# Kernel tuning notes

Measured on AMD Instinct MI355X. Metric: run time of the kernel, lower is better.

Reference implementation:

```python
import jax, jax.numpy as jnp
import numpy as np

B, L = 2, 2048
D_MODEL = 1024; D_STATE = 128; D_CONV = 4; EXPAND = 2; HEADDIM = 64
D_HALF = D_MODEL // 2
D_INNER = EXPAND * D_HALF           # 1024
NHEADS = D_INNER // HEADDIM         # 16
CONV_DIM = D_INNER + 2 * D_STATE    # 1280 (x, B, C share the depthwise conv)
D_IN_PROJ = 2 * D_INNER + 2 * D_STATE + NHEADS  # 2320 (z, xBC, dt)
EPS = 1e-5


def _rmsnorm(x, w):
    return x * jax.lax.rsqrt(jnp.mean(x * x, axis=-1, keepdims=True) + EPS) * w


def _mamba2(u, in_w, conv_w, conv_b, dt_bias, A_log, D, gnorm_w, outp_w):
    """Mamba2 block (ngroups=1, rmsnorm gated, no proj biases), u: [b,l,D_HALF]."""
    b, l, _ = u.shape
    zxbcdt = u @ in_w.T                                # [b,l,D_IN_PROJ]
    z = zxbcdt[..., :D_INNER]
    xBC = zxbcdt[..., D_INNER:D_INNER + CONV_DIM]
    dt = zxbcdt[..., D_INNER + CONV_DIM:]              # [b,l,h]
    # causal depthwise conv1d (kernel D_CONV) + silu
    xp = jnp.pad(xBC, ((0, 0), (D_CONV - 1, 0), (0, 0)))
    conv = conv_b + sum(xp[:, k:k + l, :] * conv_w[:, k] for k in range(D_CONV))
    xBC = jax.nn.silu(conv)
    x = xBC[..., :D_INNER]
    Bm = xBC[..., D_INNER:D_INNER + D_STATE]           # [b,l,n]
    Cm = xBC[..., D_INNER + D_STATE:]                  # [b,l,n]
    dt = jax.nn.softplus(dt + dt_bias)                 # [b,l,h]
    A = -jnp.exp(A_log)                                # [h]
    xh = x.reshape(b, l, NHEADS, HEADDIM)              # [b,l,h,p]
    dA = jnp.exp(dt * A)                               # [b,l,h]
    dtx = dt[..., None] * xh                           # [b,l,h,p]

    def step(h, inp):
        dA_t, dtx_t, B_t, C_t = inp
        h = dA_t[:, :, None, None] * h + jnp.einsum('bhp,bn->bhpn', dtx_t, B_t)
        return h, jnp.einsum('bhpn,bn->bhp', h, C_t)

    h0 = jnp.zeros((b, NHEADS, HEADDIM, D_STATE), u.dtype)
    xs = (jnp.moveaxis(dA, 1, 0), jnp.moveaxis(dtx, 1, 0),
          jnp.moveaxis(Bm, 1, 0), jnp.moveaxis(Cm, 1, 0))
    _, ys = jax.lax.scan(step, h0, xs)                 # ys: [l,b,h,p]
    y = jnp.moveaxis(ys, 0, 1) + xh * D[None, None, :, None]
    y = y.reshape(b, l, D_INNER) * jax.nn.silu(z)      # gate, then gated RMSNorm
    y = _rmsnorm(y, gnorm_w)
    return y @ outp_w.T                                # [b,l,D_HALF]


def _forward(x, norm_w, op_w, op_b,
             f_in_w, f_conv_w, f_conv_b, f_dt_bias, f_A_log, f_D, f_gnorm_w, f_outp_w,
             b_in_w, b_conv_w, b_conv_b, b_dt_bias, b_A_log, b_D, b_gnorm_w, b_outp_w):
    xn = _rmsnorm(x, norm_w)
    x_f, x_b = xn[..., :D_HALF], xn[..., D_HALF:]
    out_f = _mamba2(x_f, f_in_w, f_conv_w, f_conv_b, f_dt_bias, f_A_log, f_D, f_gnorm_w, f_outp_w)
    out_b = jnp.flip(
        _mamba2(jnp.flip(x_b, 1), b_in_w, b_conv_w, b_conv_b, b_dt_bias, b_A_log, b_D, b_gnorm_w, b_outp_w), 1)
    out = jnp.concatenate([out_f, out_b], axis=-1) @ op_w.T + op_b
    return x + out


def _mamba_params(key, prefix):
    k = jax.random.split(key, 5)
    return {
        prefix + 'in_w': jax.random.normal(k[0], (D_IN_PROJ, D_HALF), jnp.float32) * 0.02,
        prefix + 'conv_w': jax.random.normal(k[1], (CONV_DIM, D_CONV), jnp.float32) * 0.2,
        prefix + 'conv_b': jnp.zeros((CONV_DIM,), jnp.float32),
        prefix + 'dt_bias': jax.random.normal(k[2], (NHEADS,), jnp.float32) * 0.1,
        prefix + 'A_log': jnp.log(jax.random.uniform(k[3], (NHEADS,), jnp.float32, 1.0, 16.0)),
        prefix + 'D': jnp.ones((NHEADS,), jnp.float32),
        prefix + 'gnorm_w': jnp.ones((D_INNER,), jnp.float32),
        prefix + 'outp_w': jax.random.normal(k[4], (D_HALF, D_INNER), jnp.float32) * 0.02,
    }


def setup_inputs():
    key = jax.random.key(0)
    k = jax.random.split(key, 4)
    inp = {
        'x': jax.random.normal(k[0], (B, L, D_MODEL), jnp.float32),
        'norm_w': jnp.ones((D_MODEL,), jnp.float32),
        'op_w': jax.random.normal(k[1], (D_MODEL, D_MODEL), jnp.float32) * 0.02,
        'op_b': jnp.zeros((D_MODEL,), jnp.float32),
    }
    inp.update(_mamba_params(k[2], 'f_'))
    inp.update(_mamba_params(k[3], 'b_'))
    return inp


def reference(x, norm_w, op_w, op_b,
              f_in_w, f_conv_w, f_conv_b, f_dt_bias, f_A_log, f_D, f_gnorm_w, f_outp_w,
              b_in_w, b_conv_w, b_conv_b, b_dt_bias, b_A_log, b_D, b_gnorm_w, b_outp_w):
    return _forward(x, norm_w, op_w, op_b,
                    f_in_w, f_conv_w, f_conv_b, f_dt_bias, f_A_log, f_D, f_gnorm_w, f_outp_w,
                    b_in_w, b_conv_w, b_conv_b, b_dt_bias, b_A_log, b_D, b_gnorm_w, b_outp_w)
```

## Files before the change

### kernel.cpp

```cpp
#include <hip/hip_runtime.h>
#include <math.h>

#define L_SEQ   2048
#define NBATCH  2
#define DMODEL  1024
#define DHALF   512
#define DINNER  1024
#define DSTATE  128
#define NHEADS  16
#define HEADDIM 64
#define CONVDIM 1280
#define DINPROJ 2320
#define ROWS    4096
#define NPADIN  2432

#define QCH     64
#define NCH     (L_SEQ / QCH)

typedef __attribute__((ext_vector_type(8))) short bf16x8;
typedef __attribute__((ext_vector_type(4))) float f32x4;

union US8 { uint4 q; unsigned short s[8]; };
union US4 { uint2 q; unsigned short s[4]; };

__device__ __forceinline__ float siluf(float v){ return v / (1.f + expf(-v)); }
__device__ __forceinline__ float softplusf(float v){ return v > 20.f ? v : log1pf(expf(v)); }
__device__ __forceinline__ unsigned short f2bf(float f){
  union { float f; unsigned u; } x; x.f = f;
  unsigned r = (x.u + 0x7fffu + ((x.u >> 16) & 1u)) >> 16;
  return (unsigned short)r;
}
__device__ __forceinline__ float bf2f(unsigned short u){
  union { unsigned u; float f; } x; x.u = ((unsigned)u) << 16; return x.f;
}
__device__ __forceinline__ void gload16(const void* g, void* l){
  __builtin_amdgcn_global_load_lds((const __attribute__((address_space(1))) void*)g,
                                   (__attribute__((address_space(3))) void*)l, 16, 0, 0);
}
__device__ __forceinline__ int kx(int row){ return ((row ^ (row >> 3)) & 7) << 3; }

__device__ __forceinline__ float blockReduceSum256(float v, float* red){
  #pragma unroll
  for (int o = 32; o > 0; o >>= 1) v += __shfl_xor(v, o);
  int wid = threadIdx.x >> 6, lane = threadIdx.x & 63;
  if (lane == 0) red[wid] = v;
  __syncthreads();
  return red[0] + red[1] + red[2] + red[3];
}

__global__ void rmsnorm_split_kernel(const float* __restrict__ x, const float* __restrict__ nw,
                                     unsigned short* __restrict__ uf, unsigned short* __restrict__ ub){
  __shared__ float red[4];
  int row = blockIdx.x;
  int tid = threadIdx.x;
  float4 v4 = *(const float4*)(x + (size_t)row*DMODEL + tid*4);
  float ss = v4.x*v4.x + v4.y*v4.y + v4.z*v4.z + v4.w*v4.w;
  ss = blockReduceSum256(ss, red);
  float scale = rsqrtf(ss * (1.f/DMODEL) + 1e-5f);
  int t = row & (L_SEQ-1);
  int fliprow = (row ^ t) | (L_SEQ-1-t);
  float4 w4 = *(const float4*)(nw + tid*4);
  US4 o;
  o.s[0] = f2bf(v4.x*scale*w4.x);
  o.s[1] = f2bf(v4.y*scale*w4.y);
  o.s[2] = f2bf(v4.z*scale*w4.z);
  o.s[3] = f2bf(v4.w*scale*w4.w);
  int d = tid*4;
  if (d < DHALF) *(uint2*)&uf[(size_t)row*DHALF + d] = o.q;
  else           *(uint2*)&ub[(size_t)fliprow*DHALF + (d - DHALF)] = o.q;
}

__global__ void wconv_all_kernel(const float* __restrict__ s0, const float* __restrict__ s1,
                                 const float* __restrict__ s2, const float* __restrict__ s3,
                                 const float* __restrict__ s4,
                                 unsigned short* __restrict__ d0, unsigned short* __restrict__ d1,
                                 unsigned short* __restrict__ d2, unsigned short* __restrict__ d3,
                                 unsigned short* __restrict__ d4){
  const int S01 = NPADIN*DHALF;
  const int S23 = DHALF*DINNER;
  const int S4  = DMODEL*DMODEL;
  int idx = blockIdx.x*256 + threadIdx.x;
  if (idx < S01){
    int row = idx >> 9;
    d0[idx] = (row < DINPROJ) ? f2bf(s0[idx]) : (unsigned short)0;
    return;
  }
  idx -= S01;
  if (idx < S01){
    int row = idx >> 9;
    d1[idx] = (row < DINPROJ) ? f2bf(s1[idx]) : (unsigned short)0;
    return;
  }
  idx -= S01;
  if (idx < S23){ d2[idx] = f2bf(s2[idx]); return; }
  idx -= S23;
  if (idx < S23){ d3[idx] = f2bf(s3[idx]); return; }
  idx -= S23;
  if (idx < S4){ d4[idx] = f2bf(s4[idx]); }
}

__global__ __launch_bounds__(256) void gemm_bf16_kernel(
    const unsigned short* __restrict__ A0, const unsigned short* __restrict__ A1, int lda,
    const unsigned short* __restrict__ W0, const unsigned short* __restrict__ W1,
    float* __restrict__ Cf, int ldc,
    const float* __restrict__ bias, const float* __restrict__ res,
    unsigned short* __restrict__ O0a, unsigned short* __restrict__ O0b, int ld0,
    unsigned short* __restrict__ O1a, unsigned short* __restrict__ O1b, int n1, int ld1,
    float* __restrict__ O2a, float* __restrict__ O2b, int n2, int ld2,
    int coff1, int flip1,
    int M, int Nreal, int K){
  __shared__ unsigned short As[2][128*32];
  __shared__ unsigned short Bs[2][128*32];
  int bid = (blockIdx.z*gridDim.y + blockIdx.y)*gridDim.x + blockIdx.x;
  int nwg = gridDim.x*gridDim.y*gridDim.z;
  int s = bid;
  if ((nwg & 7) == 0){
    int cpx = nwg >> 3;
    s = (bid & 7)*cpx + (bid >> 3);
  }
  int bx = s % gridDim.x;
  int tmp = s / gridDim.x;
  int by = tmp % gridDim.y;
  int dir = tmp / gridDim.y;

  const unsigned short* A = dir ? A1 : A0;
  const unsigned short* W = dir ? W1 : W0;
  unsigned short* O0 = dir ? O0b : O0a;
  unsigned short* O1 = dir ? O1b : O1a;
  float* O2 = dir ? O2b : O2a;
  int coff = dir ? coff1 : 0;
  int flip = dir ? flip1 : 0;

  int bm = by*128, bn = bx*128;
  int tid = threadIdx.x;
  int lane = tid & 63;
  int wave = tid >> 6;
  int wm = (wave >> 1) * 64, wn = (wave & 1) * 64;
  int l15 = lane & 15, lhi = lane >> 4;
  f32x4 acc[4][4];
  #pragma unroll
  for (int i = 0; i < 4; i++)
    #pragma unroll
    for (int j = 0; j < 4; j++)
      acc[i][j] = (f32x4){0.f,0.f,0.f,0.f};

  auto stage = [&](int bufi, int k0){
    #pragma unroll
    for (int j = 0; j < 2; j++){
      int f = j*256 + tid;
      int row = f >> 2, c8 = (f & 3) * 8;
      gload16(A + (size_t)(bm+row)*lda + k0 + c8, &As[bufi][f*8]);
      gload16(W + (size_t)(bn+row)*K   + k0 + c8, &Bs[bufi][f*8]);
    }
  };

  stage(0, 0);
  __syncthreads();
  int cur = 0;
  for (int k0 = 0; k0 < K; k0 += 32){
    if (k0 + 32 < K) stage(cur ^ 1, k0 + 32);
    bf16x8 af[4], bfr[4];
    #pragma unroll
    for (int i = 0; i < 4; i++){
      af[i]  = *(const bf16x8*)&As[cur][(wm + i*16 + l15)*32 + lhi*8];
      bfr[i] = *(const bf16x8*)&Bs[cur][(wn + i*16 + l15)*32 + lhi*8];
    }
    #pragma unroll
    for (int i = 0; i < 4; i++)
      #pragma unroll
      for (int j = 0; j < 4; j++)
        acc[i][j] = __builtin_amdgcn_mfma_f32_16x16x32_bf16(af[i], bfr[j], acc[i][j], 0, 0, 0);
    __syncthreads();
    cur ^= 1;
  }
  #pragma unroll
  for (int i = 0; i < 4; i++){
    #pragma unroll
    for (int r = 0; r < 4; r++){
      int m = bm + wm + i*16 + lhi*4 + r;
      int mo = m;
      if (flip){ int t = m & (L_SEQ-1); mo = (m ^ t) | (L_SEQ-1-t); }
      #pragma unroll
      for (int j = 0; j < 4; j++){
        int n = bn + wn + j*16 + l15;
        if (n < Nreal){
          float v = acc[i][j][r];
          if (bias) v += bias[n];
          if (res)  v += res[(size_t)mo*ldc + coff + n];
          if (Cf)            Cf[(size_t)mo*ldc + coff + n] = v;
          else if (n < n1)   O0[(size_t)mo*ld0 + coff + n] = f2bf(v);
          else if (n < n2)   O1[(size_t)mo*ld1 + (n - n1)] = f2bf(v);
          else               O2[(size_t)mo*ld2 + (n - n2)] = v;
        }
      }
    }
  }
}

__global__ void conv_silu_kernel(const unsigned short* __restrict__ xbcf, const unsigned short* __restrict__ xbcb,
                                 const float* __restrict__ cwf, const float* __restrict__ cbf,
                                 const float* __restrict__ cwb, const float* __restrict__ cbb,
                                 unsigned short* __restrict__ cvf, unsigned short* __restrict__ cvb){
  int row = blockIdx.x; int dir = blockIdx.y;
  int tid = threadIdx.x;
  if (tid >= 160) return;
  const unsigned short* xbc = dir ? xbcb : xbcf;
  const float* cw = dir ? cwb : cwf;
  const float* cb = dir ? cbb : cbf;
  unsigned short* cv = dir ? cvb : cvf;
  int t = row & (L_SEQ-1);
  int c0 = tid*8;
  const unsigned short* base = xbc + (size_t)row*CONVDIM + c0;
  US8 u3, u2, u1, u0;
  u3.q = *(const uint4*)base;
  u2.q = (t >= 1) ? *(const uint4*)(base - CONVDIM)   : (uint4){0,0,0,0};
  u1.q = (t >= 2) ? *(const uint4*)(base - 2*CONVDIM) : (uint4){0,0,0,0};
  u0.q = (t >= 3) ? *(const uint4*)(base - 3*CONVDIM) : (uint4){0,0,0,0};
  US8 o;
  #pragma unroll
  for (int j = 0; j < 8; j++){
    float4 w = *(const float4*)&cw[(c0+j)*4];
    float v = cb[c0+j];
    v += bf2f(u3.s[j])*w.w + bf2f(u2.s[j])*w.z + bf2f(u1.s[j])*w.y + bf2f(u0.s[j])*w.x;
    o.s[j] = f2bf(siluf(v));
  }
  *(uint4*)&cv[(size_t)row*CONVDIM + c0] = o.q;
}

__global__ void dtcum_kernel(const float* __restrict__ drf, const float* __restrict__ drb,
                             const float* __restrict__ dbf, const float* __restrict__ alf,
                             const float* __restrict__ dbb, const float* __restrict__ alb,
                             float* __restrict__ dtf, float* __restrict__ dtb,
                             float* __restrict__ acs){
  int tid = threadIdx.x;
  int wid = blockIdx.x*4 + (tid >> 6);
  int tau = tid & 63;
  int c = wid & 31, dbh = wid >> 5;
  int h = dbh & 15, b = (dbh >> 4) & 1, dir = dbh >> 5;
  const float* dr = dir ? drb : drf;
  size_t row = (size_t)b*L_SEQ + c*QCH + tau;
  float raw = dr[row*NHEADS + h];
  float bias = (dir ? dbb : dbf)[h];
  float dtv = softplusf(raw + bias);
  float a = -expf((dir ? alb : alf)[h]);
  (dir ? dtb : dtf)[row*NHEADS + h] = dtv;
  float v = dtv * a;
  #pragma unroll
  for (int off = 1; off < 64; off <<= 1){
    float u = __shfl_up(v, off);
    if (tau >= off) v += u;
  }
  acs[(size_t)dbh*L_SEQ + c*QCH + tau] = v;
}

__global__ __launch_bounds__(256) void gemm_g_kernel(
    const unsigned short* __restrict__ cvf, const unsigned short* __restrict__ cvb,
    float* __restrict__ G){
  int c = blockIdx.x, db = blockIdx.y;
  int b = db & 1, dir = db >> 1;
  const unsigned short* cv = dir ? cvb : cvf;
  float* Gp = G + ((size_t)(db*32 + c))*4096;
  int tid = threadIdx.x, lane = tid & 63, w = tid >> 6;
  int l15 = lane & 15, lhi = lane >> 4;
  __shared__ unsigned short sB[64*128];
  __shared__ unsigned short sC[64*128];
  size_t r0 = (size_t)b*L_SEQ + (size_t)c*QCH;
  #pragma unroll
  for (int k = 0; k < 4; k++){
    int cid = k*256 + tid;
    int row = cid >> 4, slot = cid & 15;
    US8 ub, uc;
    ub.q = *(const uint4*)&cv[(r0+row)*CONVDIM + DINNER + slot*8];
    uc.q = *(const uint4*)&cv[(r0+row)*CONVDIM + DINNER + DSTATE + slot*8];
    *(uint4*)&sB[row*128 + (slot*8 ^ kx(row))] = ub.q;
    *(uint4*)&sC[row*128 + (slot*8 ^ kx(row))] = uc.q;
  }
  __syncthreads();
  int t0 = w*16;
  bf16x8 af[4];
  #pragma unroll
  for (int ks = 0; ks < 4; ks++){
    int r = t0 + l15;
    af[ks] = *(const bf16x8*)&sC[r*128 + ((ks*32 + lhi*8) ^ kx(r))];
  }
  f32x4 acc[4];
  #pragma unroll
  for (int j = 0; j < 4; j++) acc[j] = (f32x4){0.f,0.f,0.f,0.f};
  #pragma unroll
  for (int j = 0; j < 4; j++){
    #pragma unroll
    for (int ks = 0; ks < 4; ks++){
      int r = j*16 + l15;
      bf16x8 wf = *(const bf16x8*)&sB[r*128 + ((ks*32 + lhi*8) ^ kx(r))];
      acc[j] = __builtin_amdgcn_mfma_f32_16x16x32_bf16(af[ks], wf, acc[j], 0, 0, 0);
    }
  }
  #pragma unroll
  for (int j = 0; j < 4; j++)
    #pragma unroll
    for (int r = 0; r < 4; r++)
      Gp[(t0 + lhi*4 + r)*64 + j*16 + l15] = acc[j][r];
}

__global__ __launch_bounds__(256) void intra_kernel(
    const unsigned short* __restrict__ cvf, const unsigned short* __restrict__ cvb,
    const float* __restrict__ dtf, const float* __restrict__ dtb,
    const float* __restrict__ acs, const float* __restrict__ G,
    float* __restrict__ yf, float* __restrict__ yb,
    unsigned short* __restrict__ S16f, unsigned short* __restrict__ S16b){
  int c = blockIdx.x, dbh = blockIdx.y;
  int h = dbh & 15, b = (dbh >> 4) & 1, dir = dbh >> 5;
  const unsigned short* cv = dir ? cvb : cvf;
  const float* dtp = dir ? dtb : dtf;
  float* y = dir ? yb : yf;
  unsigned short* S16 = dir ? S16b : S16f;
  const float* Gp = G + ((size_t)((dir*2+b)*32 + c))*4096;
  int tid = threadIdx.x, lane = tid & 63, w = tid >> 6;
  int l15 = lane & 15, lhi = lane >> 4;

  __shared__ unsigned short sGh [64*64];
  __shared__ unsigned short sDxT[64*64];
  __shared__ unsigned short sBwT[128*64];
  __shared__ float a_sh[QCH], dt_sh[QCH];

  size_t r0 = (size_t)b*L_SEQ + (size_t)c*QCH;
  if (tid < 64){
    a_sh[tid]  = acs[(size_t)dbh*L_SEQ + c*QCH + tid];
    dt_sh[tid] = dtp[(r0 + tid)*NHEADS + h];
  }
  __syncthreads();
  float a63 = a_sh[63];
  #pragma unroll
  for (int k = 0; k < 2; k++){
    int cid = k*256 + tid;
    int s = cid >> 3, p0 = (cid & 7)*8;
    US8 u; u.q = *(const uint4*)&cv[(r0+s)*CONVDIM + h*HEADDIM + p0];
    float d = dt_sh[s];
    #pragma unroll
    for (int j = 0; j < 8; j++){
      int p = p0 + j;
      sDxT[p*64 + (s ^ kx(p))] = f2bf(bf2f(u.s[j]) * d);
    }
  }
  #pragma unroll
  for (int k = 0; k < 4; k++){
    int cid = k*256 + tid;
    int s = cid >> 4, n0 = (cid & 15)*8;
    US8 u; u.q = *(const uint4*)&cv[(r0+s)*CONVDIM + DINNER + n0];
    float wv = expf(a63 - a_sh[s]);
    #pragma unroll
    for (int j = 0; j < 8; j++){
      int n = n0 + j;
      sBwT[n*64 + (s ^ kx(n))] = f2bf(bf2f(u.s[j]) * wv);
    }
  }
  #pragma unroll
  for (int k = 0; k < 4; k++){
    int f = k*256 + tid;
    int t = f >> 4, s0 = (f & 15)*4;
    float4 g = *(const float4*)&Gp[t*64 + s0];
    float at = a_sh[t];
    float v0 = (s0+0 <= t) ? g.x*expf(at - a_sh[s0+0]) : 0.f;
    float v1 = (s0+1 <= t) ? g.y*expf(at - a_sh[s0+1]) : 0.f;
    float v2 = (s0+2 <= t) ? g.z*expf(at - a_sh[s0+2]) : 0.f;
    float v3 = (s0+3 <= t) ? g.w*expf(at - a_sh[s0+3]) : 0.f;
    int addr = t*64 + (s0 ^ kx(t));
    *(unsigned*)&sGh[addr]     = (unsigned)f2bf(v0) | ((unsigned)f2bf(v1) << 16);
    *(unsigned*)&sGh[addr + 2] = (unsigned)f2bf(v2) | ((unsigned)f2bf(v3) << 16);
  }
  __syncthreads();

  int t0 = w*16;
  bf16x8 aY[2], aS[2];
  #pragma unroll
  for (int ks = 0; ks < 2; ks++){
    int rg = t0 + l15;
    aY[ks] = *(const bf16x8*)&sGh [rg*64 + ((ks*32 + lhi*8) ^ kx(rg))];
    aS[ks] = *(const bf16x8*)&sDxT[rg*64 + ((ks*32 + lhi*8) ^ kx(rg))];
  }
  f32x4 accY[4];
  #pragma unroll
  for (int j = 0; j < 4; j++) accY[j] = (f32x4){0.f,0.f,0.f,0.f};
  #pragma unroll
  for (int j = 0; j < 4; j++){
    #pragma unroll
    for (int ks = 0; ks < 2; ks++){
      int rp = j*16 + l15;
      bf16x8 wf = *(const bf16x8*)&sDxT[rp*64 + ((ks*32 + lhi*8) ^ kx(rp))];
      accY[j] = __builtin_amdgcn_mfma_f32_16x16x32_bf16(aY[ks], wf, accY[j], 0, 0, 0);
    }
  }
  f32x4 accS[8];
  #pragma unroll
  for (int j = 0; j < 8; j++) accS[j] = (f32x4){0.f,0.f,0.f,0.f};
  #pragma unroll
  for (int j = 0; j < 8; j++){
    #pragma unroll
    for (int ks = 0; ks < 2; ks++){
      int rn = j*16 + l15;
      bf16x8 wf = *(const bf16x8*)&sBwT[rn*64 + ((ks*32 + lhi*8) ^ kx(rn))];
      accS[j] = __builtin_amdgcn_mfma_f32_16x16x32_bf16(aS[ks], wf, accS[j], 0, 0, 0);
    }
  }
  #pragma unroll
  for (int j = 0; j < 4; j++){
    #pragma unroll
    for (int r = 0; r < 4; r++){
      int t = t0 + lhi*4 + r, p = j*16 + l15;
      y[(r0 + t)*DINNER + h*HEADDIM + p] = accY[j][r];
    }
  }
  size_t sbase = ((size_t)((b*NHEADS + h)*NCH + c))*8192;
  #pragma unroll
  for (int j = 0; j < 8; j++){
    #pragma unroll
    for (int r = 0; r < 4; r++){
      int p = t0 + lhi*4 + r, n = j*16 + l15;
      S16[sbase + p*128 + n] = f2bf(accS[j][r]);
    }
  }
}

__global__ void chunkscan_kernel(const unsigned short* __restrict__ S16f,
                                 const unsigned short* __restrict__ S16b,
                                 const float* __restrict__ acs,
                                 unsigned short* __restrict__ hin16){
  __shared__ float sa[NCH];
  int tid = threadIdx.x;
  int dbh = blockIdx.x >> 4;
  int e0 = ((blockIdx.x & 15)*256 + tid)*2;
  int bh = dbh & 31, dir = dbh >> 5;
  const unsigned short* S16 = dir ? S16b : S16f;
  if (tid < NCH) sa[tid] = expf(acs[(size_t)dbh*L_SEQ + tid*QCH + 63]);
  __syncthreads();
  float h0 = 0.f, h1 = 0.f;
  #pragma unroll 8
  for (int c = 0; c < NCH; ++c){
    size_t sidx = ((size_t)(bh*NCH + c))*8192 + e0;
    size_t hidx = ((size_t)(dbh*NCH + c))*8192 + e0;
    unsigned sv = *(const unsigned*)&S16[sidx];
    unsigned hv = (unsigned)f2bf(h0) | ((unsigned)f2bf(h1) << 16);
    *(unsigned*)&hin16[hidx] = hv;
    float ea = sa[c];
    h0 = ea*h0 + bf2f((unsigned short)(sv & 0xffff));
    h1 = ea*h1 + bf2f((unsigned short)(sv >> 16));
  }
}

__global__ __launch_bounds__(256) void inter_kernel(
    const unsigned short* __restrict__ cvf, const unsigned short* __restrict__ cvb,
    const float* __restrict__ acs, const unsigned short* __restrict__ hin16,
    const float* __restrict__ Df, const float* __restrict__ Db,
    const float* __restrict__ yf, const float* __restrict__ yb,
    unsigned short* __restrict__ ygf, unsigned short* __restrict__ ygb){
  int c = blockIdx.x, dbh = blockIdx.y;
  int h = dbh & 15, b = (dbh >> 4) & 1, dir = dbh >> 5;
  const unsigned short* cv = dir ? cvb : cvf;
  const float* y = dir ? yb : yf;
  unsigned short* yg = dir ? ygb : ygf;
  float Dh = (dir ? Db : Df)[h];
  int tid = threadIdx.x, lane = tid & 63, w = tid >> 6;
  int l15 = lane & 15, lhi = lane >> 4;
  __shared__ unsigned short sC [64*128];
  __shared__ unsigned short sHT[64*128];
  __shared__ float e_sh[QCH];
  size_t r0 = (size_t)b*L_SEQ + (size_t)c*QCH;
  size_t hbase = ((size_t)(dbh*NCH + c))*8192;
  if (tid < 64) e_sh[tid] = expf(acs[(size_t)dbh*L_SEQ + c*QCH + tid]);
  #pragma unroll
  for (int k = 0; k < 4; k++){
    int cid = k*256 + tid;
    int row = cid >> 4, slot = cid & 15;
    US8 uc, uh;
    uc.q = *(const uint4*)&cv[(r0+row)*CONVDIM + DINNER + DSTATE + slot*8];
    uh.q = *(const uint4*)&hin16[hbase + cid*8];
    *(uint4*)&sC [row*128 + (slot*8 ^ kx(row))] = uc.q;
    *(uint4*)&sHT[row*128 + (slot*8 ^ kx(row))] = uh.q;
  }
  __syncthreads();
  int t0 = w*16;
  bf16x8 af[4];
  #pragma unroll
  for (int ks = 0; ks < 4; ks++){
    int r = t0 + l15;
    af[ks] = *(const bf16x8*)&sC[r*128 + ((ks*32 + lhi*8) ^ kx(r))];
  }
  f32x4 acc[4];
  #pragma unroll
  for (int j = 0; j < 4; j++) acc[j] = (f32x4){0.f,0.f,0.f,0.f};
  #pragma unroll
  for (int j = 0; j < 4; j++){
    #pragma unroll
    for (int ks = 0; ks < 4; ks++){
      int r = j*16 + l15;
      bf16x8 wf = *(const bf16x8*)&sHT[r*128 + ((ks*32 + lhi*8) ^ kx(r))];
      acc[j] = __builtin_amdgcn_mfma_f32_16x16x32_bf16(af[ks], wf, acc[j], 0, 0, 0);
    }
  }
  #pragma unroll
  for (int j = 0; j < 4; j++){
    #pragma unroll
    for (int r = 0; r < 4; r++){
      int t = t0 + lhi*4 + r, p = j*16 + l15;
      size_t row = r0 + t;
      float xv = bf2f(cv[row*CONVDIM + h*HEADDIM + p]);
      float v = y[row*DINNER + h*HEADDIM + p] + e_sh[t]*acc[j][r] + Dh*xv;
      yg[row*DINNER + h*HEADDIM + p] = f2bf(v);
    }
  }
}

__global__ void gate_norm_kernel(unsigned short* __restrict__ ygf, unsigned short* __restrict__ ygb,
                                 const unsigned short* __restrict__ z16f, const unsigned short* __restrict__ z16b,
                                 const float* __restrict__ gwf, const float* __restrict__ gwb){
  __shared__ float red[4];
  int row = blockIdx.x; int dir = blockIdx.y;
  int tid = threadIdx.x;
  unsigned short* yg = (dir ? ygb : ygf) + (size_t)row*DINNER;
  const unsigned short* z = (dir ? z16b : z16f) + (size_t)row*DINNER;
  const float* gw = dir ? gwb : gwf;
  int d = tid*4;
  US4 uy, uz;
  uy.q = *(const uint2*)&yg[d];
  uz.q = *(const uint2*)&z[d];
  float v[4]; float ss = 0.f;
  #pragma unroll
  for (int k = 0; k < 4; k++){
    float val = bf2f(uy.s[k]) * siluf(bf2f(uz.s[k]));
    v[k] = val; ss += val*val;
  }
  ss = blockReduceSum256(ss, red);
  float scale = rsqrtf(ss*(1.f/DINNER) + 1e-5f);
  float4 w4 = *(const float4*)&gw[d];
  US4 o;
  o.s[0] = f2bf(v[0]*scale*w4.x);
  o.s[1] = f2bf(v[1]*scale*w4.y);
  o.s[2] = f2bf(v[2]*scale*w4.z);
  o.s[3] = f2bf(v[3]*scale*w4.w);
  *(uint2*)&yg[d] = o.q;
}

extern "C" void kernel_launch(void* const* d_in, const int* in_sizes, int n_in,
                              void* d_out, int out_size, void* d_ws, size_t ws_size,
                              hipStream_t stream) {
  const float* x      = (const float*)d_in[0];
  const float* norm_w = (const float*)d_in[1];
  const float* op_w   = (const float*)d_in[2];
  const float* op_b   = (const float*)d_in[3];
  const float* f_in_w    = (const float*)d_in[4];
  const float* f_conv_w  = (const float*)d_in[5];
  const float* f_conv_b  = (const float*)d_in[6];
  const float* f_dt_bias = (const float*)d_in[7];
  const float* f_A_log   = (const float*)d_in[8];
  const float* f_D       = (const float*)d_in[9];
  const float* f_gnorm_w = (const float*)d_in[10];
  const float* f_outp_w  = (const float*)d_in[11];
  const float* b_in_w    = (const float*)d_in[12];
  const float* b_conv_w  = (const float*)d_in[13];
  const float* b_conv_b  = (const float*)d_in[14];
  const float* b_dt_bias = (const float*)d_in[15];
  const float* b_A_log   = (const float*)d_in[16];
  const float* b_D       = (const float*)d_in[17];
  const float* b_gnorm_w = (const float*)d_in[18];
  const float* b_outp_w  = (const float*)d_in[19];
  float* out = (float*)d_out;

  float* ws = (float*)d_ws;
  size_t off = 0;
  unsigned short* u16f = (unsigned short*)(ws + off);
  unsigned short* u16b = u16f + (size_t)ROWS*DHALF;      off += (size_t)ROWS*DHALF;
  unsigned short* z16f = (unsigned short*)(ws + off);    off += (size_t)ROWS*DINNER/2;
  unsigned short* z16b = (unsigned short*)(ws + off);    off += (size_t)ROWS*DINNER/2;
  unsigned short* xbc16f = (unsigned short*)(ws + off);  off += (size_t)ROWS*CONVDIM/2;
  unsigned short* xbc16b = (unsigned short*)(ws + off);  off += (size_t)ROWS*CONVDIM/2;
  float* draw_f = ws + off; off += (size_t)ROWS*NHEADS;
  float* draw_b = ws + off; off += (size_t)ROWS*NHEADS;
  unsigned short* cv16f = (unsigned short*)(ws + off); off += (size_t)ROWS*CONVDIM/2;
  unsigned short* cv16b = (unsigned short*)(ws + off); off += (size_t)ROWS*CONVDIM/2;
  float* dt_f = ws + off; off += (size_t)ROWS*NHEADS;
  float* dt_b = ws + off; off += (size_t)ROWS*NHEADS;
  float* y_f  = ws + off; off += (size_t)ROWS*DINNER;
  float* y_b  = ws + off; off += (size_t)ROWS*DINNER;
  unsigned short* yg16f = (unsigned short*)(ws + off); off += (size_t)ROWS*DINNER/2;
  unsigned short* yg16b = (unsigned short*)(ws + off); off += (size_t)ROWS*DINNER/2;
  float* acs  = ws + off; off += (size_t)64*L_SEQ;
  float* G    = ws + off; off += (size_t)128*QCH*QCH;
  unsigned short* S16f = (unsigned short*)(ws + off); off += (size_t)32*NCH*8192/2;
  unsigned short* S16b = (unsigned short*)(ws + off); off += (size_t)32*NCH*8192/2;
  unsigned short* hin16 = (unsigned short*)(ws + off); off += (size_t)64*NCH*8192/2;
  unsigned short* w16_fin  = (unsigned short*)(ws + off); off += (size_t)NPADIN*DHALF/2;
  unsigned short* w16_bin  = (unsigned short*)(ws + off); off += (size_t)NPADIN*DHALF/2;
  unsigned short* w16_fout = (unsigned short*)(ws + off); off += (size_t)DHALF*DINNER/2;
  unsigned short* w16_bout = (unsigned short*)(ws + off); off += (size_t)DHALF*DINNER/2;
  unsigned short* w16_op   = (unsigned short*)(ws + off); off += (size_t)DMODEL*DMODEL/2;
  unsigned short* cat16 = z16f;

  rmsnorm_split_kernel<<<ROWS, 256, 0, stream>>>(x, norm_w, u16f, u16b);
  {
    const int TOT = 2*NPADIN*DHALF + 2*DHALF*DINNER + DMODEL*DMODEL;
    wconv_all_kernel<<<(TOT+255)/256, 256, 0, stream>>>(
        f_in_w, b_in_w, f_outp_w, b_outp_w, op_w,
        w16_fin, w16_bin, w16_fout, w16_bout, w16_op);
  }
  gemm_bf16_kernel<<<dim3(NPADIN/128, ROWS/128, 2), 256, 0, stream>>>(
      u16f, u16b, DHALF, w16_fin, w16_bin,
      nullptr, 0, nullptr, nullptr,
      z16f, z16b, DINNER,
      xbc16f, xbc16b, DINNER, CONVDIM,
      draw_f, draw_b, DINNER+CONVDIM, NHEADS,
      0, 0,
      ROWS, DINPROJ, DHALF);
  conv_silu_kernel<<<dim3(ROWS, 2), 256, 0, stream>>>(
      xbc16f, xbc16b, f_conv_w, f_conv_b, b_conv_w, b_conv_b, cv16f, cv16b);
  dtcum_kernel<<<512, 256, 0, stream>>>(
      draw_f, draw_b, f_dt_bias, f_A_log, b_dt_bias, b_A_log, dt_f, dt_b, acs);
  gemm_g_kernel<<<dim3(32, 4), 256, 0, stream>>>(cv16f, cv16b, G);
  intra_kernel<<<dim3(32, 64), 256, 0, stream>>>(cv16f, cv16b, dt_f, dt_b, acs, G,
                                                 y_f, y_b, S16f, S16b);
  chunkscan_kernel<<<1024, 256, 0, stream>>>(S16f, S16b, acs, hin16);
  inter_kernel<<<dim3(32, 64), 256, 0, stream>>>(cv16f, cv16b, acs, hin16, f_D, b_D,
                                                 y_f, y_b, yg16f, yg16b);
  gate_norm_kernel<<<dim3(ROWS, 2), 256, 0, stream>>>(
      yg16f, yg16b, z16f, z16b, f_gnorm_w, b_gnorm_w);
  gemm_bf16_kernel<<<dim3(DHALF/128, ROWS/128, 2), 256, 0, stream>>>(
      yg16f, yg16b, DINNER, w16_fout, w16_bout,
      nullptr, 0, nullptr, nullptr,
      cat16, cat16, DMODEL,
      nullptr, nullptr, 1<<30, 0,
      nullptr, nullptr, 1<<30, 0,
      DHALF, 1,
      ROWS, DHALF, DINNER);
  gemm_bf16_kernel<<<dim3(DMODEL/128, ROWS/128, 1), 256, 0, stream>>>(
      cat16, nullptr, DMODEL, w16_op, nullptr,
      out, DMODEL, op_b, x,
      nullptr, nullptr, 0,
      nullptr, nullptr, 1<<30, 0,
      nullptr, nullptr, 1<<30, 0,
      0, 0,
      ROWS, DMODEL, DMODEL);
}
```

Measured before the change: 240.9 us.

## Templatize GEMM M-tile, vectorize weight conversion, merge conv directions per block

The GEMM kernel is templated on its M tile size, and the two output-projection GEMMs use 64-row tiles so they launch twice as many workgroups. The aim is to fill the GPU better on these small-N GEMMs, at the cost of less reuse of each loaded weight tile. The weight fp32-to-bf16 conversion now handles four elements per thread with vector loads and stores. The conv+silu kernel processes both directions in one 320-thread block instead of idling 96 of 256 threads, which halves the block count and removes the wasted lanes.

Result: faster. 222.8 us (-7.5%).

```diff
diff --git a/kernel.cpp b/kernel.cpp
--- a/kernel.cpp
+++ b/kernel.cpp
@@ -79,27 +79,26 @@
   const int S01 = NPADIN*DHALF;
   const int S23 = DHALF*DINNER;
   const int S4  = DMODEL*DMODEL;
-  int idx = blockIdx.x*256 + threadIdx.x;
-  if (idx < S01){
-    int row = idx >> 9;
-    d0[idx] = (row < DINPROJ) ? f2bf(s0[idx]) : (unsigned short)0;
-    return;
-  }
-  idx -= S01;
-  if (idx < S01){
-    int row = idx >> 9;
-    d1[idx] = (row < DINPROJ) ? f2bf(s1[idx]) : (unsigned short)0;
-    return;
-  }
-  idx -= S01;
-  if (idx < S23){ d2[idx] = f2bf(s2[idx]); return; }
-  idx -= S23;
-  if (idx < S23){ d3[idx] = f2bf(s3[idx]); return; }
-  idx -= S23;
-  if (idx < S4){ d4[idx] = f2bf(s4[idx]); }
-}
-
-__global__ __launch_bounds__(256) void gemm_bf16_kernel(
+  int idx = (blockIdx.x*256 + threadIdx.x)*4;
+  const float* s; unsigned short* d; int pad_rows = 0;
+  if (idx < S01){ s = s0; d = d0; pad_rows = DINPROJ; }
+  else if ((idx -= S01) < S01){ s = s1; d = d1; pad_rows = DINPROJ; }
+  else if ((idx -= S01) < S23){ s = s2; d = d2; }
+  else if ((idx -= S23) < S23){ s = s3; d = d3; }
+  else if ((idx -= S23) < S4){ s = s4; d = d4; }
+  else return;
+  US4 o;
+  if (pad_rows && (idx >> 9) >= pad_rows){
+    o.s[0] = o.s[1] = o.s[2] = o.s[3] = 0;
+  } else {
+    float4 v = *(const float4*)&s[idx];
+    o.s[0] = f2bf(v.x); o.s[1] = f2bf(v.y); o.s[2] = f2bf(v.z); o.s[3] = f2bf(v.w);
+  }
+  *(uint2*)&d[idx] = o.q;
+}
+
+template<int TM>
+__global__ __launch_bounds__(256) void gemm_bf16_t(
     const unsigned short* __restrict__ A0, const unsigned short* __restrict__ A1, int lda,
     const unsigned short* __restrict__ W0, const unsigned short* __restrict__ W1,
     float* __restrict__ Cf, int ldc,
@@ -109,7 +108,8 @@
     float* __restrict__ O2a, float* __restrict__ O2b, int n2, int ld2,
     int coff1, int flip1,
     int M, int Nreal, int K){
-  __shared__ unsigned short As[2][128*32];
+  constexpr int MI = TM/32;
+  __shared__ unsigned short As[2][TM*32];
   __shared__ unsigned short Bs[2][128*32];
   int bid = (blockIdx.z*gridDim.y + blockIdx.y)*gridDim.x + blockIdx.x;
   int nwg = gridDim.x*gridDim.y*gridDim.z;
@@ -131,26 +131,29 @@
   int coff = dir ? coff1 : 0;
   int flip = dir ? flip1 : 0;
 
-  int bm = by*128, bn = bx*128;
+  int bm = by*TM, bn = bx*128;
   int tid = threadIdx.x;
   int lane = tid & 63;
   int wave = tid >> 6;
-  int wm = (wave >> 1) * 64, wn = (wave & 1) * 64;
+  int wm = (wave >> 1) * (TM/2), wn = (wave & 1) * 64;
   int l15 = lane & 15, lhi = lane >> 4;
-  f32x4 acc[4][4];
-  #pragma unroll
-  for (int i = 0; i < 4; i++)
+  f32x4 acc[MI][4];
+  #pragma unroll
+  for (int i = 0; i < MI; i++)
     #pragma unroll
     for (int j = 0; j < 4; j++)
       acc[i][j] = (f32x4){0.f,0.f,0.f,0.f};
 
   auto stage = [&](int bufi, int k0){
     #pragma unroll
-    for (int j = 0; j < 2; j++){
-      int f = j*256 + tid;
+    for (int f = tid; f < TM*4; f += 256){
       int row = f >> 2, c8 = (f & 3) * 8;
       gload16(A + (size_t)(bm+row)*lda + k0 + c8, &As[bufi][f*8]);
-      gload16(W + (size_t)(bn+row)*K   + k0 + c8, &Bs[bufi][f*8]);
+    }
+    #pragma unroll
+    for (int f = tid; f < 512; f += 256){
+      int row = f >> 2, c8 = (f & 3) * 8;
+      gload16(W + (size_t)(bn+row)*K + k0 + c8, &Bs[bufi][f*8]);
     }
   };
 
@@ -159,14 +162,15 @@
   int cur = 0;
   for (int k0 = 0; k0 < K; k0 += 32){
     if (k0 + 32 < K) stage(cur ^ 1, k0 + 32);
-    bf16x8 af[4], bfr[4];
-    #pragma unroll
-    for (int i = 0; i < 4; i++){
-      af[i]  = *(const bf16x8*)&As[cur][(wm + i*16 + l15)*32 + lhi*8];
-      bfr[i] = *(const bf16x8*)&Bs[cur][(wn + i*16 + l15)*32 + lhi*8];
-    }
-    #pragma unroll
-    for (int i = 0; i < 4; i++)
+    bf16x8 af[MI], bfr[4];
+    #pragma unroll
+    for (int i = 0; i < MI; i++)
+      af[i] = *(const bf16x8*)&As[cur][(wm + i*16 + l15)*32 + lhi*8];
+    #pragma unroll
+    for (int j = 0; j < 4; j++)
+      bfr[j] = *(const bf16x8*)&Bs[cur][(wn + j*16 + l15)*32 + lhi*8];
+    #pragma unroll
+    for (int i = 0; i < MI; i++)
       #pragma unroll
       for (int j = 0; j < 4; j++)
         acc[i][j] = __builtin_amdgcn_mfma_f32_16x16x32_bf16(af[i], bfr[j], acc[i][j], 0, 0, 0);
@@ -174,7 +178,7 @@
     cur ^= 1;
   }
   #pragma unroll
-  for (int i = 0; i < 4; i++){
+  for (int i = 0; i < MI; i++){
     #pragma unroll
     for (int r = 0; r < 4; r++){
       int m = bm + wm + i*16 + lhi*4 + r;
@@ -201,15 +205,16 @@
                                  const float* __restrict__ cwf, const float* __restrict__ cbf,
                                  const float* __restrict__ cwb, const float* __restrict__ cbb,
                                  unsigned short* __restrict__ cvf, unsigned short* __restrict__ cvb){
-  int row = blockIdx.x; int dir = blockIdx.y;
+  int row = blockIdx.x;
   int tid = threadIdx.x;
-  if (tid >= 160) return;
+  int dir = tid >= 160;
+  int slot = tid - dir*160;
   const unsigned short* xbc = dir ? xbcb : xbcf;
   const float* cw = dir ? cwb : cwf;
   const float* cb = dir ? cbb : cbf;
   unsigned short* cv = dir ? cvb : cvf;
   int t = row & (L_SEQ-1);
-  int c0 = tid*8;
+  int c0 = slot*8;
   const unsigned short* base = xbc + (size_t)row*CONVDIM + c0;
   US8 u3, u2, u1, u0;
   u3.q = *(const uint4*)base;
@@ -598,11 +603,11 @@
   rmsnorm_split_kernel<<<ROWS, 256, 0, stream>>>(x, norm_w, u16f, u16b);
   {
     const int TOT = 2*NPADIN*DHALF + 2*DHALF*DINNER + DMODEL*DMODEL;
-    wconv_all_kernel<<<(TOT+255)/256, 256, 0, stream>>>(
+    wconv_all_kernel<<<(TOT/4+255)/256, 256, 0, stream>>>(
         f_in_w, b_in_w, f_outp_w, b_outp_w, op_w,
         w16_fin, w16_bin, w16_fout, w16_bout, w16_op);
   }
-  gemm_bf16_kernel<<<dim3(NPADIN/128, ROWS/128, 2), 256, 0, stream>>>(
+  gemm_bf16_t<128><<<dim3(NPADIN/128, ROWS/128, 2), 256, 0, stream>>>(
       u16f, u16b, DHALF, w16_fin, w16_bin,
       nullptr, 0, nullptr, nullptr,
       z16f, z16b, DINNER,
@@ -610,7 +615,7 @@
       draw_f, draw_b, DINNER+CONVDIM, NHEADS,
       0, 0,
       ROWS, DINPROJ, DHALF);
-  conv_silu_kernel<<<dim3(ROWS, 2), 256, 0, stream>>>(
+  conv_silu_kernel<<<ROWS, 320, 0, stream>>>(
       xbc16f, xbc16b, f_conv_w, f_conv_b, b_conv_w, b_conv_b, cv16f, cv16b);
   dtcum_kernel<<<512, 256, 0, stream>>>(
       draw_f, draw_b, f_dt_bias, f_A_log, b_dt_bias, b_A_log, dt_f, dt_b, acs);
@@ -622,7 +627,7 @@
                                                  y_f, y_b, yg16f, yg16b);
   gate_norm_kernel<<<dim3(ROWS, 2), 256, 0, stream>>>(
       yg16f, yg16b, z16f, z16b, f_gnorm_w, b_gnorm_w);
-  gemm_bf16_kernel<<<dim3(DHALF/128, ROWS/128, 2), 256, 0, stream>>>(
+  gemm_bf16_t<64><<<dim3(DHALF/128, ROWS/64, 2), 256, 0, stream>>>(
       yg16f, yg16b, DINNER, w16_fout, w16_bout,
       nullptr, 0, nullptr, nullptr,
       cat16, cat16, DMODEL,
@@ -630,7 +635,7 @@
       nullptr, nullptr, 1<<30, 0,
       DHALF, 1,
       ROWS, DHALF, DINNER);
-  gemm_bf16_kernel<<<dim3(DMODEL/128, ROWS/128, 1), 256, 0, stream>>>(
+  gemm_bf16_t<64><<<dim3(DMODEL/128, ROWS/64, 1), 256, 0, stream>>>(
       cat16, nullptr, DMODEL, w16_op, nullptr,
       out, DMODEL, op_b, x,
       nullptr, nullptr, 0,
```
